# Optimization experiments

Hardware: AMD Instinct MI355X
Metric: run time of the kernel (lower is better)

The kernel has to match this reference:

```python
import jax, jax.numpy as jnp
import numpy as np

DT = 1.0       # integration timestep
THRESH = 0.5   # firing threshold (standard in this family of SNN repos)


def setup_inputs() -> dict:
    key = jax.random.key(0)
    ks = jax.random.split(key, 6)
    B, Din, Dout = 32768, 256, 512
    input_spike = jax.random.uniform(ks[0], (B, Din), dtype=jnp.float32)
    mem = jnp.zeros((B, Dout), jnp.float32)
    spike = jnp.zeros((B, Dout), jnp.float32)
    s_in = 1.0 / np.sqrt(Din)
    s_h = 1.0 / np.sqrt(Dout)
    W_dense = jax.random.uniform(ks[1], (Dout, Din), minval=-s_in, maxval=s_in, dtype=jnp.float32)
    b_dense = jax.random.uniform(ks[2], (Dout,), minval=-s_in, maxval=s_in, dtype=jnp.float32)
    W_rec = jax.random.uniform(ks[3], (Dout, Dout), minval=-s_h, maxval=s_h, dtype=jnp.float32)
    b_rec = jax.random.uniform(ks[4], (Dout,), minval=-s_h, maxval=s_h, dtype=jnp.float32)
    tau_m = 20.0 + 5.0 * jax.random.normal(ks[5], (Dout,), dtype=jnp.float32)
    return dict(input_spike=input_spike, mem=mem, spike=spike,
                W_dense=W_dense, b_dense=b_dense, W_rec=W_rec, b_rec=b_rec,
                tau_m=tau_m)


def reference(input_spike, mem, spike, W_dense, b_dense, W_rec, b_rec, tau_m):
    # d_input = dense(input_spike) + recurrent(spike)
    d_input = (jnp.einsum('bi,oi->bo', input_spike, W_dense) + b_dense
               + jnp.einsum('bh,oh->bo', spike, W_rec) + b_rec)
    # LIF neuron dynamics: exponential membrane decay, soft reset, heaviside spike
    alpha = jnp.exp(-DT / tau_m)                                   # [Dout]
    mem_new = mem * alpha + (1.0 - alpha) * d_input - THRESH * spike
    spike_new = (mem_new - THRESH > 0).astype(mem_new.dtype)
    return mem_new, spike_new
```

## Files before the change

### kernel.cpp

```cpp
#include <hip/hip_runtime.h>
#include <math.h>

typedef short  short8  __attribute__((ext_vector_type(8)));
typedef short  short4v __attribute__((ext_vector_type(4)));
typedef float  f32x4   __attribute__((ext_vector_type(4)));

#define BATCH 32768
#define DIN   256
#define DOUT  512
#define BM    128
#define BN    64

#define WS_FLAGS 0
#define WS_WD2   4096
#define WS_WR2   (4096 + 262144)
#define WS_X2    (266240 + 524288)

__device__ __forceinline__ short f2bf(float v) {
    unsigned u = __float_as_uint(v);
    u += 0x7fffu + ((u >> 16) & 1u);
    return (short)(u >> 16);
}

__global__ __launch_bounds__(256) void prepass_kernel(
    const float* __restrict__ SPK, const float* __restrict__ X,
    const float* __restrict__ Wd,  const float* __restrict__ Wr,
    int* __restrict__ flags, short* __restrict__ X2,
    short* __restrict__ Wd2, short* __restrict__ Wr2)
{
    const int b   = blockIdx.x;
    const int tid = threadIdx.x;

    {
        unsigned bits = 0;
        const f32x4* p = (const f32x4*)SPK + (size_t)b * 2048;
#pragma unroll
        for (int j = 0; j < 8; j++) {
            f32x4 v = p[tid + j * 256];
            bits |= __float_as_uint(v[0]) | __float_as_uint(v[1])
                  | __float_as_uint(v[2]) | __float_as_uint(v[3]);
        }
        if (__any(bits != 0) && (tid & 63) == 0)
            atomicOr(&flags[b >> 3], 1);
    }

    {
        const f32x4* src = (const f32x4*)X + (size_t)b * 1024;
        short4v*     dst = (short4v*)X2   + (size_t)b * 1024;
#pragma unroll
        for (int j = 0; j < 4; j++) {
            f32x4 v = src[tid + j * 256];
            dst[tid + j * 256] = (short4v){f2bf(v[0]), f2bf(v[1]),
                                           f2bf(v[2]), f2bf(v[3])};
        }
    }

    {
        int idx = b * 256 + tid;
        if (idx < 32768) {
            f32x4 v = ((const f32x4*)Wd)[idx];
            ((short4v*)Wd2)[idx] = (short4v){f2bf(v[0]), f2bf(v[1]),
                                             f2bf(v[2]), f2bf(v[3])};
        } else if (idx < 98304) {
            int k = idx - 32768;
            f32x4 v = ((const f32x4*)Wr)[k];
            ((short4v*)Wr2)[k] = (short4v){f2bf(v[0]), f2bf(v[1]),
                                           f2bf(v[2]), f2bf(v[3])};
        }
    }
}

__global__ __launch_bounds__(256, 3) void spike_rnn_lif_kernel(
    const short* __restrict__ X2,
    const float* __restrict__ MEM,
    const float* __restrict__ SPK,
    const short* __restrict__ Wd2,
    const float* __restrict__ bd,
    const short* __restrict__ Wr2,
    const float* __restrict__ br,
    const float* __restrict__ tau,
    const int*   __restrict__ flags,
    float* __restrict__ out)
{
    __shared__ float sT[64 * 68];

    const int tid  = threadIdx.x;
    const int lane = tid & 63;
    const int w    = tid >> 6;
    const int wm   = w & 1;
    const int wn   = w >> 1;

    const int L    = blockIdx.x;
    const int bm   = ((L >> 6) << 3) + (L & 7);
    const int bn   = (L >> 3) & 7;
    const int m0   = bm * BM;
    const int n0   = bn * BN;
    const int col  = lane & 15;
    const int quad = lane >> 4;

    const bool has_spk = (flags[bm] != 0);

    const int c4   = tid & 15;
    const int ncol = n0 + c4 * 4;
    f32x4 mv0[4], mv1[4];
#pragma unroll
    for (int it = 0; it < 4; it++) {
        int r2 = (tid + it * 256) >> 4;
        mv0[it] = __builtin_nontemporal_load(
                      (const f32x4*)(MEM + (size_t)(m0 + r2) * DOUT + ncol));
        mv1[it] = __builtin_nontemporal_load(
                      (const f32x4*)(MEM + (size_t)(m0 + 64 + r2) * DOUT + ncol));
    }

    f32x4 acc[4][2];
#pragma unroll
    for (int i = 0; i < 4; i++)
#pragma unroll
        for (int j = 0; j < 2; j++)
            acc[i][j] = (f32x4){0.f, 0.f, 0.f, 0.f};

    {
        const short* Abase = X2  + (size_t)(m0 + wm * 64 + col) * DIN + quad * 8;
        const short* Bbase = Wd2 + (size_t)(n0 + wn * 32 + col) * DIN + quad * 8;

#define LOAD_AB(kk, aa, bb)                                                   \
        do {                                                                  \
            int k_ = (kk) * 32;                                               \
            _Pragma("unroll")                                                 \
            for (int t = 0; t < 4; t++)                                       \
                aa[t] = *(const short8*)(Abase + (size_t)t * 16 * DIN + k_);  \
            _Pragma("unroll")                                                 \
            for (int t = 0; t < 2; t++)                                       \
                bb[t] = *(const short8*)(Bbase + (size_t)t * 16 * DIN + k_);  \
        } while (0)

#define MFMA_AB(aa, bb)                                                       \
        do {                                                                  \
            _Pragma("unroll")                                                 \
            for (int i = 0; i < 4; i++)                                       \
                _Pragma("unroll")                                             \
                for (int j = 0; j < 2; j++)                                   \
                    acc[i][j] = __builtin_amdgcn_mfma_f32_16x16x32_bf16(      \
                        aa[i], bb[j], acc[i][j], 0, 0, 0);                    \
        } while (0)

        short8 a0[4], b0[2], a1[4], b1[2];
        LOAD_AB(0, a0, b0);
#pragma unroll
        for (int kp = 0; kp < 4; kp++) {
            LOAD_AB(2 * kp + 1, a1, b1);
            MFMA_AB(a0, b0);
            if (kp < 3) LOAD_AB(2 * kp + 2, a0, b0);
            MFMA_AB(a1, b1);
        }
#undef LOAD_AB
    }

    if (has_spk) {
        const float* Abase = SPK + (size_t)(m0 + wm * 64 + col) * DOUT + quad * 8;
        const short* Bbase = Wr2 + (size_t)(n0 + wn * 32 + col) * DOUT + quad * 8;
#pragma unroll 4
        for (int ks = 0; ks < 16; ks++) {
            int k = ks * 32;
            short8 a[4], b[2];
#pragma unroll
            for (int t = 0; t < 4; t++) {
                const float* ap = Abase + (size_t)t * 16 * DOUT + k;
                f32x4 lo = *(const f32x4*)ap;
                f32x4 hi = *(const f32x4*)(ap + 4);
                a[t] = (short8){f2bf(lo[0]), f2bf(lo[1]), f2bf(lo[2]), f2bf(lo[3]),
                                f2bf(hi[0]), f2bf(hi[1]), f2bf(hi[2]), f2bf(hi[3])};
            }
#pragma unroll
            for (int t = 0; t < 2; t++)
                b[t] = *(const short8*)(Bbase + (size_t)t * 16 * DOUT + k);
            MFMA_AB(a, b);
        }
    }
#undef MFMA_AB

    float al[4], oma[4], bs[4];
#pragma unroll
    for (int q = 0; q < 4; q++) {
        al[q]  = expf(-1.0f / tau[ncol + q]);
        oma[q] = 1.0f - al[q];
        bs[q]  = bd[ncol + q] + br[ncol + q];
    }

#pragma unroll
    for (int c = 0; c < 2; c++) {
        if (c) __syncthreads();
        if (wm == c) {
#pragma unroll
            for (int j = 0; j < 2; j++)
#pragma unroll
                for (int i = 0; i < 4; i++)
#pragma unroll
                    for (int rr = 0; rr < 4; rr++)
                        sT[(i * 16 + quad * 4 + rr) * 68 + wn * 32 + j * 16 + col]
                            = acc[i][j][rr];
        }
        __syncthreads();
#pragma unroll
        for (int it = 0; it < 4; it++) {
            int p   = tid + it * 256;
            int r2  = p >> 4;
            int row = m0 + c * 64 + r2;
            f32x4 d  = *(const f32x4*)(sT + r2 * 68 + c4 * 4);
            f32x4 mv = c ? mv1[it] : mv0[it];
            f32x4 sv = has_spk ? *(const f32x4*)(SPK + (size_t)row * DOUT + ncol)
                               : (f32x4){0.f, 0.f, 0.f, 0.f};
            f32x4 mn, sp;
#pragma unroll
            for (int q = 0; q < 4; q++) {
                mn[q] = mv[q] * al[q] + oma[q] * (d[q] + bs[q]) - 0.5f * sv[q];
                sp[q] = (mn[q] - 0.5f > 0.0f) ? 1.0f : 0.0f;
            }
            __builtin_nontemporal_store(mn,
                (f32x4*)(out + (size_t)row * DOUT + ncol));
            __builtin_nontemporal_store(sp,
                (f32x4*)(out + (size_t)BATCH * DOUT + (size_t)row * DOUT + ncol));
        }
    }
}

extern "C" void kernel_launch(void* const* d_in, const int* in_sizes, int n_in,
                              void* d_out, int out_size, void* d_ws, size_t ws_size,
                              hipStream_t stream) {
    const float* X   = (const float*)d_in[0];
    const float* MEM = (const float*)d_in[1];
    const float* SPK = (const float*)d_in[2];
    const float* Wd  = (const float*)d_in[3];
    const float* bd  = (const float*)d_in[4];
    const float* Wr  = (const float*)d_in[5];
    const float* br  = (const float*)d_in[6];
    const float* tau = (const float*)d_in[7];

    char*  ws    = (char*)d_ws;
    int*   flags = (int*)  (ws + WS_FLAGS);
    short* Wd2   = (short*)(ws + WS_WD2);
    short* Wr2   = (short*)(ws + WS_WR2);
    short* X2    = (short*)(ws + WS_X2);

    hipMemsetAsync(flags, 0, 256 * sizeof(int), stream);
    prepass_kernel<<<2048, 256, 0, stream>>>(SPK, X, Wd, Wr, flags, X2, Wd2, Wr2);

    spike_rnn_lif_kernel<<<2048, 256, 0, stream>>>(X2, MEM, SPK, Wd2, bd, Wr2, br,
                                                   tau, flags, (float*)d_out);
}
```

Before: 303.7 us.

## Stage dense GEMM operands into swizzled LDS via direct global-to-LDS loads

The dense-layer GEMM used to read A (X2) and B (Wd2) fragments straight from global memory into registers. It now copies them into a 48KB XOR-swizzled shared-memory tile with global_load_lds in two K halves, then reads the MFMA fragments from LDS. The aim is to replace strided per-lane global loads with coalesced bulk copies and bank-conflict-free LDS reads. In exchange it adds several barriers and serialises the load and compute of each half, and the larger LDS footprint may lower occupancy below the launch-bounds target of 3 blocks per CU.

```diff
diff --git a/kernel.cpp b/kernel.cpp
--- a/kernel.cpp
+++ b/kernel.cpp
@@ -20,6 +20,12 @@
     unsigned u = __float_as_uint(v);
     u += 0x7fffu + ((u >> 16) & 1u);
     return (short)(u >> 16);
+}
+
+__device__ __forceinline__ void gload_lds16(const void* g, void* l) {
+    __builtin_amdgcn_global_load_lds(
+        (const __attribute__((address_space(1))) unsigned int*)g,
+        (__attribute__((address_space(3))) unsigned int*)l, 16, 0, 0);
 }
 
 __global__ __launch_bounds__(256) void prepass_kernel(
@@ -82,7 +88,8 @@
     const int*   __restrict__ flags,
     float* __restrict__ out)
 {
-    __shared__ float sT[64 * 68];
+    __shared__ __align__(16) char smem[49152];
+    float* sT = (float*)smem;
 
     const int tid  = threadIdx.x;
     const int lane = tid & 63;
@@ -100,6 +107,30 @@
 
     const bool has_spk = (flags[bm] != 0);
 
+    const int l16 = lane & 15, lr4 = lane >> 4;
+
+#define STAGE(c0)                                                             \
+    do {                                                                      \
+        _Pragma("unroll")                                                     \
+        for (int i = 0; i < 8; i++) {                                         \
+            int seg = w * 8 + i;                     \
+            int r   = seg * 4 + lr4;                                          \
+            const char* src = (const char*)X2 + (size_t)(m0 + r) * 512        \
+                            + (c0) * 256 + ((l16 * 16) ^ ((r & 7) << 4));     \
+            gload_lds16(src, smem + seg * 1024);                              \
+        }                                                                     \
+        _Pragma("unroll")                                                     \
+        for (int i = 0; i < 4; i++) {                                         \
+            int seg = w * 4 + i;                                              \
+            int r   = seg * 4 + lr4;                                          \
+            const char* src = (const char*)Wd2 + (size_t)(n0 + r) * 512       \
+                            + (c0) * 256 + ((l16 * 16) ^ ((r & 7) << 4));     \
+            gload_lds16(src, smem + 32768 + seg * 1024);                      \
+        }                                                                     \
+    } while (0)
+
+    STAGE(0);
+
     const int c4   = tid & 15;
     const int ncol = n0 + c4 * 4;
     f32x4 mv0[4], mv1[4];
@@ -119,42 +150,50 @@
         for (int j = 0; j < 2; j++)
             acc[i][j] = (f32x4){0.f, 0.f, 0.f, 0.f};
 
-    {
-        const short* Abase = X2  + (size_t)(m0 + wm * 64 + col) * DIN + quad * 8;
-        const short* Bbase = Wd2 + (size_t)(n0 + wn * 32 + col) * DIN + quad * 8;
-
-#define LOAD_AB(kk, aa, bb)                                                   \
-        do {                                                                  \
-            int k_ = (kk) * 32;                                               \
+    const int swz  = (col & 7) << 4;
+    const int arow = wm * 64 + col;
+    const int brow = wn * 32 + col;
+
+#define DSLOAD(kk, aa, bb)                                                    \
+    do {                                                                      \
+        int ko = (quad * 16 + (kk) * 64) ^ swz;                               \
+        _Pragma("unroll")                                                     \
+        for (int t = 0; t < 4; t++)                                           \
+            aa[t] = *(const short8*)(smem + (arow + t * 16) * 256 + ko);      \
+        _Pragma("unroll")                                                     \
+        for (int t = 0; t < 2; t++)                                           \
+            bb[t] = *(const short8*)(smem + 32768 + (brow + t * 16) * 256 + ko); \
+    } while (0)
+
+#define MFMA_AB(aa, bb)                                                       \
+    do {                                                                      \
+        _Pragma("unroll")                                                     \
+        for (int i = 0; i < 4; i++)                                           \
             _Pragma("unroll")                                                 \
-            for (int t = 0; t < 4; t++)                                       \
-                aa[t] = *(const short8*)(Abase + (size_t)t * 16 * DIN + k_);  \
-            _Pragma("unroll")                                                 \
-            for (int t = 0; t < 2; t++)                                       \
-                bb[t] = *(const short8*)(Bbase + (size_t)t * 16 * DIN + k_);  \
-        } while (0)
-
-#define MFMA_AB(aa, bb)                                                       \
-        do {                                                                  \
-            _Pragma("unroll")                                                 \
-            for (int i = 0; i < 4; i++)                                       \
-                _Pragma("unroll")                                             \
-                for (int j = 0; j < 2; j++)                                   \
-                    acc[i][j] = __builtin_amdgcn_mfma_f32_16x16x32_bf16(      \
-                        aa[i], bb[j], acc[i][j], 0, 0, 0);                    \
-        } while (0)
-
-        short8 a0[4], b0[2], a1[4], b1[2];
-        LOAD_AB(0, a0, b0);
-#pragma unroll
-        for (int kp = 0; kp < 4; kp++) {
-            LOAD_AB(2 * kp + 1, a1, b1);
-            MFMA_AB(a0, b0);
-            if (kp < 3) LOAD_AB(2 * kp + 2, a0, b0);
-            MFMA_AB(a1, b1);
-        }
-#undef LOAD_AB
-    }
+            for (int j = 0; j < 2; j++)                                       \
+                acc[i][j] = __builtin_amdgcn_mfma_f32_16x16x32_bf16(          \
+                    aa[i], bb[j], acc[i][j], 0, 0, 0);                        \
+    } while (0)
+
+    short8 a0[4], b0[2], a1[4], b1[2];
+
+    __syncthreads();
+    DSLOAD(0, a0, b0);
+    DSLOAD(1, a1, b1); MFMA_AB(a0, b0);
+    DSLOAD(2, a0, b0); MFMA_AB(a1, b1);
+    DSLOAD(3, a1, b1); MFMA_AB(a0, b0);
+    MFMA_AB(a1, b1);
+    __syncthreads();
+
+    STAGE(1);
+    __syncthreads();
+    DSLOAD(0, a0, b0);
+    DSLOAD(1, a1, b1); MFMA_AB(a0, b0);
+    DSLOAD(2, a0, b0); MFMA_AB(a1, b1);
+    DSLOAD(3, a1, b1); MFMA_AB(a0, b0);
+    MFMA_AB(a1, b1);
+#undef DSLOAD
+#undef STAGE
 
     if (has_spk) {
         const float* Abase = SPK + (size_t)(m0 + wm * 64 + col) * DOUT + quad * 8;
@@ -186,6 +225,8 @@
         oma[q] = 1.0f - al[q];
         bs[q]  = bd[ncol + q] + br[ncol + q];
     }
+
+    __syncthreads();
 
 #pragma unroll
     for (int c = 0; c < 2; c++) {
```

Result: faster. 272.6 us, median of 2 (-10.3%).
